# Kernel optimization log

Hardware: AMD Instinct MI355X
Metric: run time of the kernel (lower is better)

Reference implementation:

```python
import jax, jax.numpy as jnp
import numpy as np

DIM = 384
HEADS = 6
HEAD_DIM = DIM // HEADS
HIDDEN = int(DIM * 4.0)
SCALE = HEAD_DIM ** (-0.5)
EPS = 1e-5


def _layernorm(x, w, b):
    m = jnp.mean(x, axis=-1, keepdims=True)
    v = jnp.var(x, axis=-1, keepdims=True)
    return (x - m) * jax.lax.rsqrt(v + EPS) * w + b


def _mlp(x, fc1_w, fc1_b, fc2_w, fc2_b):
    h = jnp.einsum('bnc,hc->bnh', x, fc1_w) + fc1_b
    h = jax.nn.gelu(h, approximate=False)  # torch nn.GELU default = exact erf
    return jnp.einsum('bnh,ch->bnc', h, fc2_w) + fc2_b


def _attn_block(q, k, v, proj_w, proj_b):
    # q:[B,H,Q,D] k,v:[B,H,K,D]
    attn = jnp.einsum('bhqd,bhkd->bhqk', q, k) * SCALE
    attn = jax.nn.softmax(attn, axis=-1)
    o = jnp.einsum('bhqk,bhkd->bhqd', attn, v)
    B, H, Q, D = o.shape
    o = o.transpose(0, 2, 1, 3).reshape(B, Q, H * D)
    return jnp.einsum('bqc,oc->bqo', o, proj_w) + proj_b


def setup_inputs() -> dict:
    key = jax.random.key(0)
    ks = jax.random.split(key, 10)
    s = 0.02
    return {
        'x': jax.random.normal(ks[0], (4, 2048, DIM), jnp.float32),
        'y': jax.random.normal(ks[1], (4, 256, DIM), jnp.float32),
        'norm1_w': jnp.ones((DIM,), jnp.float32),
        'norm1_b': jnp.zeros((DIM,), jnp.float32),
        'norm2_w': jnp.ones((DIM,), jnp.float32),
        'norm2_b': jnp.zeros((DIM,), jnp.float32),
        'qkv_w': jax.random.normal(ks[2], (3 * DIM, DIM), jnp.float32) * s,
        'proj_w': jax.random.normal(ks[3], (DIM, DIM), jnp.float32) * s,
        'proj_b': jnp.zeros((DIM,), jnp.float32),
        'fc1_w': jax.random.normal(ks[4], (HIDDEN, DIM), jnp.float32) * s,
        'fc1_b': jnp.zeros((HIDDEN,), jnp.float32),
        'fc2_w': jax.random.normal(ks[5], (DIM, HIDDEN), jnp.float32) * s,
        'fc2_b': jnp.zeros((DIM,), jnp.float32),
    }


def reference(x, y, norm1_w, norm1_b, norm2_w, norm2_b, qkv_w,
              proj_w, proj_b, fc1_w, fc1_b, fc2_w, fc2_b):
    B, N, C = x.shape
    L = y.shape[1]
    nx = _layernorm(x, norm1_w, norm1_b)
    ny = _layernorm(y, norm1_w, norm1_b)
    cat = jnp.concatenate([nx, ny], axis=1)  # [B, N+L, C]
    qkv = jnp.einsum('bnc,oc->bno', cat, qkv_w)
    qkv = qkv.reshape(B, N + L, 3, HEADS, HEAD_DIM).transpose(2, 0, 3, 1, 4)
    q, k, v = qkv[0], qkv[1], qkv[2]  # each [B,H,N+L,D]
    # cross: y-queries attend over all N+L keys
    y_att = _attn_block(q[:, :, N:], k, v, proj_w, proj_b)
    # self: x-queries attend over first N keys only
    x_att = _attn_block(q[:, :, :N], k[:, :, :N], v[:, :, :N], proj_w, proj_b)
    new_x = x + x_att
    new_y = y + y_att
    new_x = new_x + _mlp(_layernorm(new_x, norm2_w, norm2_b), fc1_w, fc1_b, fc2_w, fc2_b)
    new_y = new_y + _mlp(_layernorm(new_y, norm2_w, norm2_b), fc1_w, fc1_b, fc2_w, fc2_b)
    return (new_x, new_y)
```

## Files before the change

kernel.cpp:

```cpp
#include <hip/hip_runtime.h>
#include <hip/hip_bf16.h>
#include <math.h>

#define B_   4
#define NX   2048
#define NY   256
#define T_   2304
#define NTOK 9216
#define DIM  384
#define NH   6
#define HD   64
#define HID  1536
#define QKV3 1152
#define QK2  768

typedef __attribute__((ext_vector_type(8))) short bf16x8;
typedef __attribute__((ext_vector_type(4))) float f32x4;

__device__ __forceinline__ float b2f(unsigned short u) {
  union { unsigned int i; float f; } x; x.i = ((unsigned int)u) << 16; return x.f;
}
__device__ __forceinline__ unsigned short f2b(float f) {
  union { float f; unsigned int i; } x; x.f = f;
  unsigned int r = x.i + 0x7fffu + ((x.i >> 16) & 1u);
  return (unsigned short)(r >> 16);
}
__device__ __forceinline__ unsigned int pack2(float a, float b) {
  return (unsigned int)f2b(a) | ((unsigned int)f2b(b) << 16);
}
__device__ __forceinline__ unsigned int cvtpk(float a, float b) {
  unsigned int r;
  asm("v_cvt_pk_bf16_f32 %0, %1, %2" : "=v"(r) : "v"(a), "v"(b));
  return r;
}
__device__ __forceinline__ float ldin(const void* p, size_t i, int isbf) {
  return isbf ? b2f(((const unsigned short*)p)[i]) : ((const float*)p)[i];
}

#if defined(__has_builtin)
#if __has_builtin(__builtin_amdgcn_global_load_lds)
#define HAS_GLL 1
#endif
#endif

__device__ __forceinline__ void stage16(const unsigned short* g, unsigned short* l) {
#ifdef HAS_GLL
  __builtin_amdgcn_global_load_lds(
      (const __attribute__((address_space(1))) unsigned int*)g,
      (__attribute__((address_space(3))) unsigned int*)l, 16, 0, 0);
#else
  *(uint4*)(l + (threadIdx.x & 63) * 8) = *(const uint4*)g;
#endif
}

__global__ void detect_kernel(const unsigned short* __restrict__ qw,
                              int* __restrict__ flag) {
  int lane = threadIdx.x;
  int bad = 0;
  #pragma unroll
  for (int j = 0; j < 8; j++) {
    unsigned short u = qw[2 * (lane + 64 * j)];
    int e = (u >> 7) & 0xff;
    bad += (e >= 134) ? 1 : 0;
  }
  #pragma unroll
  for (int off = 32; off > 0; off >>= 1) bad += __shfl_xor(bad, off);
  if (lane == 0) *flag = (bad < 64) ? 1 : 0;
}

__global__ __launch_bounds__(256) void convert4_kernel(
    const void* __restrict__ s0, const void* __restrict__ s1,
    const void* __restrict__ s2, const void* __restrict__ s3,
    unsigned short* __restrict__ d0, const int* __restrict__ flagp) {
  int isbf = *flagp;
  int i = (blockIdx.x * 256 + threadIdx.x) * 8;
  const void* src; int off;
  if (i < 442368)       { src = s0; off = 0; }
  else if (i < 589824)  { src = s1; off = 442368; }
  else if (i < 1179648) { src = s2; off = 589824; }
  else                  { src = s3; off = 1179648; }
  int li = i - off;
  if (isbf) {
    *(uint4*)(d0 + i) = *(const uint4*)((const unsigned short*)src + li);
  } else {
    const float* s = (const float*)src + li;
    unsigned int w[4];
    #pragma unroll
    for (int j = 0; j < 4; j++) w[j] = pack2(s[2 * j], s[2 * j + 1]);
    *(uint4*)(d0 + i) = make_uint4(w[0], w[1], w[2], w[3]);
  }
}

__global__ __launch_bounds__(256) void ln1_kernel(
    const void* __restrict__ x, const void* __restrict__ y,
    const void* __restrict__ w, const void* __restrict__ bsh,
    const int* __restrict__ flagp, unsigned short* __restrict__ out)
{
  int isbf = *flagp;
  int token = blockIdx.x * 4 + (threadIdx.x >> 6);
  int lane  = threadIdx.x & 63;
  int bb = token / T_;
  int t  = token - bb * T_;
  const void* src = (t < NX) ? x : y;
  size_t base = (t < NX) ? ((size_t)bb * NX + t) * DIM
                         : ((size_t)bb * NY + (t - NX)) * DIM;
  float v[6];
  float s = 0.f, s2 = 0.f;
  #pragma unroll
  for (int k = 0; k < 6; k++) {
    v[k] = ldin(src, base + lane + 64 * k, isbf);
    s += v[k]; s2 += v[k] * v[k];
  }
  #pragma unroll
  for (int off = 32; off > 0; off >>= 1) {
    s  += __shfl_xor(s, off);
    s2 += __shfl_xor(s2, off);
  }
  float mean = s * (1.f / DIM);
  float var  = s2 * (1.f / DIM) - mean * mean;
  float rs = rsqrtf(var + 1e-5f);
  unsigned short* dst = out + (size_t)token * DIM;
  #pragma unroll
  for (int k = 0; k < 6; k++) {
    int c = lane + 64 * k;
    dst[c] = f2b((v[k] - mean) * rs * ldin(w, c, isbf) + ldin(bsh, c, isbf));
  }
}

__global__ __launch_bounds__(256) void ln2_kernel(
    const float* __restrict__ in, const void* __restrict__ w,
    const void* __restrict__ bsh, const int* __restrict__ flagp,
    unsigned short* __restrict__ out)
{
  int isbf = *flagp;
  int token = blockIdx.x * 4 + (threadIdx.x >> 6);
  int lane  = threadIdx.x & 63;
  const float* src = in + (size_t)token * DIM;
  float v[6];
  float s = 0.f, s2 = 0.f;
  #pragma unroll
  for (int k = 0; k < 6; k++) {
    v[k] = src[lane + 64 * k];
    s += v[k]; s2 += v[k] * v[k];
  }
  #pragma unroll
  for (int off = 32; off > 0; off >>= 1) {
    s  += __shfl_xor(s, off);
    s2 += __shfl_xor(s2, off);
  }
  float mean = s * (1.f / DIM);
  float var  = s2 * (1.f / DIM) - mean * mean;
  float rs = rsqrtf(var + 1e-5f);
  unsigned short* dst = out + (size_t)token * DIM;
  #pragma unroll
  for (int k = 0; k < 6; k++) {
    int c = lane + 64 * k;
    dst[c] = f2b((v[k] - mean) * rs * ldin(w, c, isbf) + ldin(bsh, c, isbf));
  }
}

template <int EPI, int KT>
__global__ __launch_bounds__(256) void gemm_mfma(
    const unsigned short* __restrict__ A, const unsigned short* __restrict__ Bw,
    const void* __restrict__ bias,
    const void* __restrict__ rx, const void* __restrict__ ry,
    const float* __restrict__ rf,
    unsigned short* __restrict__ outb, float* __restrict__ resf,
    void* __restrict__ outd, unsigned short* __restrict__ vTp,
    const int* __restrict__ flagp, int N)
{
  constexpr int NT = KT / 32;
  __shared__ unsigned short As[2][128 * 32];
  __shared__ unsigned short Bs[2][128 * 32];
  const int tid  = threadIdx.x;
  const int wave = tid >> 6, lane = tid & 63;
  const int g = lane >> 4, qq = lane & 15;
  const int gx = gridDim.x;
  const int flat = blockIdx.x + gx * blockIdx.y;
  const int cpx = (gx * gridDim.y) >> 3;
  const int L = (flat & 7) * cpx + (flat >> 3);
  const int n0 = (L % gx) * 128, m0 = (L / gx) * 128;
  const int wm = (wave & 1) * 64, wn = (wave >> 1) * 64;

  f32x4 z = {0.f, 0.f, 0.f, 0.f};
  f32x4 acc[4][4];
  #pragma unroll
  for (int i = 0; i < 4; i++)
    #pragma unroll
    for (int j = 0; j < 4; j++) acc[i][j] = z;

  const int lrow = lane >> 2;
  const int lkx  = (((lane & 3) ^ ((lane >> 3) & 3)) * 8);
  const int rsw  = (qq >> 1) & 3;

  auto STG = [&](int t, int bi_) {
    int k0_ = t * 32;
    #pragma unroll
    for (int r = 0; r < 2; r++) {
      int rbase = wave * 32 + r * 16;
      stage16(A  + (size_t)(m0 + rbase + lrow) * KT + k0_ + lkx,
              &As[bi_][rbase * 32]);
      stage16(Bw + (size_t)(n0 + rbase + lrow) * KT + k0_ + lkx,
              &Bs[bi_][rbase * 32]);
    }
  };
  auto COMPUTE = [&](int bi_) {
    const unsigned short* as = As[bi_];
    const unsigned short* bs = Bs[bi_];
    bf16x8 af[4], bf[4];
    #pragma unroll
    for (int i = 0; i < 4; i++)
      af[i] = *(const bf16x8*)&as[(wm + i * 16 + qq) * 32 + ((g ^ rsw) * 8)];
    #pragma unroll
    for (int j = 0; j < 4; j++)
      bf[j] = *(const bf16x8*)&bs[(wn + j * 16 + qq) * 32 + ((g ^ rsw) * 8)];
    __builtin_amdgcn_s_setprio(1);
    #pragma unroll
    for (int i = 0; i < 4; i++)
      #pragma unroll
      for (int j = 0; j < 4; j++)
        acc[i][j] = __builtin_amdgcn_mfma_f32_16x16x32_bf16(
            af[i], bf[j], acc[i][j], 0, 0, 0);
    __builtin_amdgcn_s_setprio(0);
  };
  #define GSYNC() do { \
    asm volatile("s_waitcnt vmcnt(0)" ::: "memory"); \
    __builtin_amdgcn_s_barrier(); } while (0)

  STG(0, 0);
  GSYNC();
  #pragma unroll 1
  for (int t = 0; t + 2 < NT; t += 2) {
    STG(t + 1, 1);
    COMPUTE(0);
    GSYNC();
    STG(t + 2, 0);
    COMPUTE(1);
    GSYNC();
  }
  STG(NT - 1, 1);
  COMPUTE(0);
  GSYNC();
  COMPUTE(1);
  #undef GSYNC

  if (EPI == 0 && n0 >= 768) {
    #pragma unroll
    for (int i = 0; i < 4; i++) {
      int mb = m0 + wm + i * 16 + g * 4;
      int bb = mb / T_;
      int t  = mb - bb * T_;
      #pragma unroll
      for (int j = 0; j < 4; j++) {
        int n = n0 + wn + j * 16 + qq;
        int hh = (n - 768) >> 6, dd = (n - 768) & 63;
        uint2 pk;
        pk.x = pack2(acc[i][j][0], acc[i][j][1]);
        pk.y = pack2(acc[i][j][2], acc[i][j][3]);
        *(uint2*)(vTp + ((size_t)(bb * NH + hh) * HD + dd) * T_ + t) = pk;
      }
    }
    return;
  }

  int isbf = (EPI == 0) ? 1 : *flagp;
  float qs = (EPI == 0 && n0 < 384) ? 0.18033688011f : 1.f;
  const bool kswz = (EPI == 0) && (n0 >= 384);
  #pragma unroll
  for (int i = 0; i < 4; i++) {
    #pragma unroll
    for (int r = 0; r < 4; r++) {
      int m = m0 + wm + i * 16 + g * 4 + r;
      int bb = m / T_;
      int t  = m - bb * T_;
      int ms = kswz ? ((m & ~31) | ((g & 1) << 4) | ((i & 1) << 3) |
                       ((g >> 1) << 2) | r)
                    : m;
      #pragma unroll
      for (int j = 0; j < 4; j++) {
        int n = n0 + wn + j * 16 + qq;
        float v = acc[i][j][r];
        if (EPI == 0) {
          outb[(size_t)ms * QK2 + n] = f2b(v * qs);
        } else if (EPI == 1) {
          float resv = (t < NX)
              ? ldin(rx, ((size_t)bb * NX + t) * DIM + n, isbf)
              : ldin(ry, ((size_t)bb * NY + (t - NX)) * DIM + n, isbf);
          resf[(size_t)m * DIM + n] = v + ldin(bias, n, isbf) + resv;
        } else if (EPI == 2) {
          float h = v + ldin(bias, n, isbf);
          outb[(size_t)m * N + n] =
              f2b(0.5f * h * (1.f + erff(h * 0.70710678118654752f)));
        } else {
          float rr = v + ldin(bias, n, isbf) + rf[(size_t)m * DIM + n];
          size_t oi = (t < NX)
              ? ((size_t)bb * NX + t) * DIM + n
              : (size_t)B_ * NX * DIM + ((size_t)bb * NY + (t - NX)) * DIM + n;
          if (isbf) ((unsigned short*)outd)[oi] = f2b(rr);
          else      ((float*)outd)[oi] = rr;
        }
      }
    }
  }
}

__global__ __launch_bounds__(256) void attn_mfma(
    const unsigned short* __restrict__ qk, const unsigned short* __restrict__ vT,
    unsigned short* __restrict__ att)
{
  __shared__ float Ob[64][68];
  __shared__ float Lb[64];
  const int tid = threadIdx.x;
  const int wave = tid >> 6, lane = tid & 63;
  const int g = lane >> 4, qq = lane & 15;
  const int flat = blockIdx.x;
  const int L = (flat & 7) * 108 + (flat >> 3);
  const int bx = L % 36;
  const int hb = L / 36;
  const int h = hb % NH, b = hb / NH;
  const int self = (bx < 32);
  const int qtok0 = self ? bx * 64 : NX + (bx - 32) * 64;
  const int kvbeg = wave * (self ? 512 : 576);
  const int ntile = self ? 16 : 18;

  bf16x8 qa[4][2];
  #pragma unroll
  for (int f = 0; f < 4; f++) {
    size_t qrow = (size_t)(b * T_ + qtok0 + f * 16 + qq) * QK2 + h * HD;
    qa[f][0] = *(const bf16x8*)(qk + qrow + g * 8);
    qa[f][1] = *(const bf16x8*)(qk + qrow + 32 + g * 8);
  }
  const unsigned short* kb = qk + (size_t)b * T_ * QK2 + DIM + h * HD;
  const unsigned short* vb = vT + (size_t)(b * NH + h) * HD * T_;

  f32x4 z = {0.f, 0.f, 0.f, 0.f};
  f32x4 ot[4][4];
  #pragma unroll
  for (int f = 0; f < 4; f++)
    #pragma unroll
    for (int dt = 0; dt < 4; dt++) ot[f][dt] = z;
  float lsum[4] = {0.f, 0.f, 0.f, 0.f};

  uint4 kc[4];
  #pragma unroll
  for (int c = 0; c < 2; c++)
    #pragma unroll
    for (int hh = 0; hh < 2; hh++)
      kc[c * 2 + hh] =
          *(const uint4*)(kb + (size_t)(kvbeg + c * 16 + qq) * QK2 + hh * 32 + g * 8);
  uint4 vc[4];
  #pragma unroll
  for (int dt = 0; dt < 4; dt++)
    vc[dt] = *(const uint4*)(vb + (size_t)(dt * 16 + qq) * T_ + kvbeg + g * 8);

  int kt = kvbeg;
  for (int it = 0; it < ntile; it++, kt += 32) {
    f32x4 s[4][2];
    __builtin_amdgcn_s_setprio(1);
    #pragma unroll
    for (int f = 0; f < 4; f++) {
      s[f][0] = __builtin_amdgcn_mfma_f32_16x16x32_bf16(
          *(const bf16x8*)&kc[0], qa[f][0], z, 0, 0, 0);
      s[f][0] = __builtin_amdgcn_mfma_f32_16x16x32_bf16(
          *(const bf16x8*)&kc[1], qa[f][1], s[f][0], 0, 0, 0);
      s[f][1] = __builtin_amdgcn_mfma_f32_16x16x32_bf16(
          *(const bf16x8*)&kc[2], qa[f][0], z, 0, 0, 0);
      s[f][1] = __builtin_amdgcn_mfma_f32_16x16x32_bf16(
          *(const bf16x8*)&kc[3], qa[f][1], s[f][1], 0, 0, 0);
    }
    __builtin_amdgcn_s_setprio(0);
    if (it + 1 < ntile) {
      int ktn = kt + 32;
      #pragma unroll
      for (int c = 0; c < 2; c++)
        #pragma unroll
        for (int hh = 0; hh < 2; hh++)
          kc[c * 2 + hh] = *(const uint4*)(
              kb + (size_t)(ktn + c * 16 + qq) * QK2 + hh * 32 + g * 8);
    }

    #pragma unroll
    for (int f = 0; f < 4; f++) {
      float pv[8];
      #pragma unroll
      for (int c = 0; c < 2; c++)
        #pragma unroll
        for (int r = 0; r < 4; r++)
          pv[c * 4 + r] = exp2f(s[f][c][r]);
      lsum[f] += ((pv[0] + pv[1]) + (pv[2] + pv[3])) +
                 ((pv[4] + pv[5]) + (pv[6] + pv[7]));
      union { unsigned int w[4]; bf16x8 v; } bq;
      bq.w[0] = cvtpk(pv[0], pv[1]);
      bq.w[1] = cvtpk(pv[2], pv[3]);
      bq.w[2] = cvtpk(pv[4], pv[5]);
      bq.w[3] = cvtpk(pv[6], pv[7]);
      __builtin_amdgcn_s_setprio(1);
      #pragma unroll
      for (int dt = 0; dt < 4; dt++)
        ot[f][dt] = __builtin_amdgcn_mfma_f32_16x16x32_bf16(
            *(const bf16x8*)&vc[dt], bq.v, ot[f][dt], 0, 0, 0);
      __builtin_amdgcn_s_setprio(0);
    }

    if (it + 1 < ntile) {
      int ktn = kt + 32;
      #pragma unroll
      for (int dt = 0; dt < 4; dt++)
        vc[dt] = *(const uint4*)(vb + (size_t)(dt * 16 + qq) * T_ + ktn + g * 8);
    }
  }

  #pragma unroll
  for (int f = 0; f < 4; f++) {
    lsum[f] += __shfl_xor(lsum[f], 16);
    lsum[f] += __shfl_xor(lsum[f], 32);
  }

  #pragma unroll
  for (int w = 0; w < 4; w++) {
    if (wave == w) {
      if (w == 0) {
        #pragma unroll
        for (int f = 0; f < 4; f++) {
          #pragma unroll
          for (int dt = 0; dt < 4; dt++)
            *(f32x4*)&Ob[f * 16 + qq][dt * 16 + g * 4] = ot[f][dt];
          if (g == 0) Lb[f * 16 + qq] = lsum[f];
        }
      } else {
        #pragma unroll
        for (int f = 0; f < 4; f++) {
          #pragma unroll
          for (int dt = 0; dt < 4; dt++) {
            f32x4 cur = *(const f32x4*)&Ob[f * 16 + qq][dt * 16 + g * 4];
            #pragma unroll
            for (int r = 0; r < 4; r++) cur[r] += ot[f][dt][r];
            *(f32x4*)&Ob[f * 16 + qq][dt * 16 + g * 4] = cur;
          }
          if (g == 0) Lb[f * 16 + qq] += lsum[f];
        }
      }
    }
    __syncthreads();
  }

  int q = tid >> 2, ds = (tid & 3) * 16;
  float inv = 1.f / Lb[q];
  float o[16];
  #pragma unroll
  for (int j = 0; j < 16; j += 4) {
    f32x4 a = *(const f32x4*)&Ob[q][ds + j];
    #pragma unroll
    for (int r = 0; r < 4; r++) o[j + r] = a[r] * inv;
  }
  unsigned int w[8];
  #pragma unroll
  for (int j = 0; j < 8; j++) w[j] = pack2(o[2 * j], o[2 * j + 1]);
  size_t orow = (size_t)(b * T_ + qtok0 + q) * DIM + h * HD + ds;
  *(uint4*)(att + orow)     = make_uint4(w[0], w[1], w[2], w[3]);
  *(uint4*)(att + orow + 8) = make_uint4(w[4], w[5], w[6], w[7]);
}

extern "C" void kernel_launch(void* const* d_in, const int* in_sizes, int n_in,
                              void* d_out, int out_size, void* d_ws, size_t ws_size,
                              hipStream_t stream)
{
  (void)in_sizes; (void)n_in; (void)out_size; (void)ws_size;
  const void* x    = d_in[0];
  const void* y    = d_in[1];
  const void* n1w  = d_in[2];
  const void* n1b  = d_in[3];
  const void* n2w  = d_in[4];
  const void* n2b  = d_in[5];
  const void* qkvw = d_in[6];
  const void* pw   = d_in[7];
  const void* pb   = d_in[8];
  const void* f1w  = d_in[9];
  const void* f1b  = d_in[10];
  const void* f2w  = d_in[11];
  const void* f2bp = d_in[12];

  unsigned short* wsu = (unsigned short*)d_ws;
  int* flag = (int*)d_ws;
  unsigned short* wts    = wsu + 128;
  unsigned short* qkvw_b = wts;
  unsigned short* pw_b   = wts + 442368;
  unsigned short* f1w_b  = wts + 589824;
  unsigned short* f2w_b  = wts + 1179648;
  unsigned short* catln  = wsu + 1769600;
  unsigned short* qkvb2  = wsu + 5308544;
  unsigned short* attb   = wsu + 12386432;
  unsigned short* vT     = wsu + 15925376;
  unsigned short* hbuf   = qkvb2;
  float*          resb   = (float*)d_ws + 9732160;

  detect_kernel<<<1, 64, 0, stream>>>((const unsigned short*)qkvw, flag);
  convert4_kernel<<<864, 256, 0, stream>>>(qkvw, pw, f1w, f2w, wts, flag);

  ln1_kernel<<<NTOK / 4, 256, 0, stream>>>(x, y, n1w, n1b, flag, catln);
  gemm_mfma<0, DIM><<<dim3(QKV3 / 128, NTOK / 128), 256, 0, stream>>>(
      catln, qkvw_b, nullptr, nullptr, nullptr, nullptr, qkvb2, nullptr,
      nullptr, vT, flag, QKV3);
  attn_mfma<<<dim3(864), 256, 0, stream>>>(qkvb2, vT, attb);
  gemm_mfma<1, DIM><<<dim3(DIM / 128, NTOK / 128), 256, 0, stream>>>(
      attb, pw_b, pb, x, y, nullptr, nullptr, resb, nullptr, nullptr,
      flag, DIM);
  ln2_kernel<<<NTOK / 4, 256, 0, stream>>>(resb, n2w, n2b, flag, catln);
  gemm_mfma<2, DIM><<<dim3(HID / 128, NTOK / 128), 256, 0, stream>>>(
      catln, f1w_b, f1b, nullptr, nullptr, nullptr, hbuf, nullptr, nullptr,
      nullptr, flag, HID);
  gemm_mfma<3, HID><<<dim3(DIM / 128, NTOK / 128), 256, 0, stream>>>(
      hbuf, f2w_b, f2bp, nullptr, nullptr, resb, nullptr, nullptr, d_out,
      nullptr, flag, DIM);
}
```

Baseline: 319.1 us.

## Replace LDS-staged GEMM with direct global-to-register triple-buffered fragment loads

The GEMM kernel drops shared-memory staging and barriers. Each wave now loads its MFMA fragments directly from global memory into registers, with a three-deep software pipeline. The block tile shrinks from 128x128 to 128x64, with each wave owning 32 rows across all 64 columns, and the grids double in the N dimension. This removes LDS traffic and synchronization, but every wave now reloads the shared B fragments from global/L2, so data reuse within the block is lost.

Measured after the change: 409.3 us. 28.3% more time.

```diff
diff --git a/kernel.cpp b/kernel.cpp
--- a/kernel.cpp
+++ b/kernel.cpp
@@ -35,22 +35,6 @@
 }
 __device__ __forceinline__ float ldin(const void* p, size_t i, int isbf) {
   return isbf ? b2f(((const unsigned short*)p)[i]) : ((const float*)p)[i];
-}
-
-#if defined(__has_builtin)
-#if __has_builtin(__builtin_amdgcn_global_load_lds)
-#define HAS_GLL 1
-#endif
-#endif
-
-__device__ __forceinline__ void stage16(const unsigned short* g, unsigned short* l) {
-#ifdef HAS_GLL
-  __builtin_amdgcn_global_load_lds(
-      (const __attribute__((address_space(1))) unsigned int*)g,
-      (__attribute__((address_space(3))) unsigned int*)l, 16, 0, 0);
-#else
-  *(uint4*)(l + (threadIdx.x & 63) * 8) = *(const uint4*)g;
-#endif
 }
 
 __global__ void detect_kernel(const unsigned short* __restrict__ qw,
@@ -170,8 +154,6 @@
     const int* __restrict__ flagp, int N)
 {
   constexpr int NT = KT / 32;
-  __shared__ unsigned short As[2][128 * 32];
-  __shared__ unsigned short Bs[2][128 * 32];
   const int tid  = threadIdx.x;
   const int wave = tid >> 6, lane = tid & 63;
   const int g = lane >> 4, qq = lane & 15;
@@ -179,80 +161,65 @@
   const int flat = blockIdx.x + gx * blockIdx.y;
   const int cpx = (gx * gridDim.y) >> 3;
   const int L = (flat & 7) * cpx + (flat >> 3);
-  const int n0 = (L % gx) * 128, m0 = (L / gx) * 128;
-  const int wm = (wave & 1) * 64, wn = (wave >> 1) * 64;
+  const int n0 = (L % gx) * 64, m0 = (L / gx) * 128;
+  const int wm = wave * 32;
 
   f32x4 z = {0.f, 0.f, 0.f, 0.f};
-  f32x4 acc[4][4];
-  #pragma unroll
-  for (int i = 0; i < 4; i++)
+  f32x4 acc[2][4];
+  #pragma unroll
+  for (int i = 0; i < 2; i++)
     #pragma unroll
     for (int j = 0; j < 4; j++) acc[i][j] = z;
 
-  const int lrow = lane >> 2;
-  const int lkx  = (((lane & 3) ^ ((lane >> 3) & 3)) * 8);
-  const int rsw  = (qq >> 1) & 3;
-
-  auto STG = [&](int t, int bi_) {
-    int k0_ = t * 32;
-    #pragma unroll
-    for (int r = 0; r < 2; r++) {
-      int rbase = wave * 32 + r * 16;
-      stage16(A  + (size_t)(m0 + rbase + lrow) * KT + k0_ + lkx,
-              &As[bi_][rbase * 32]);
-      stage16(Bw + (size_t)(n0 + rbase + lrow) * KT + k0_ + lkx,
-              &Bs[bi_][rbase * 32]);
-    }
+  unsigned int aoff[2], boff[4];
+  #pragma unroll
+  for (int i = 0; i < 2; i++)
+    aoff[i] = (unsigned int)(m0 + wm + i * 16 + qq) * KT + g * 8;
+  #pragma unroll
+  for (int j = 0; j < 4; j++)
+    boff[j] = (unsigned int)(n0 + j * 16 + qq) * KT + g * 8;
+
+  auto LDF = [&](uint4 (&fa)[2], uint4 (&fb)[4], int t) {
+    const int ke = t * 32;
+    #pragma unroll
+    for (int i = 0; i < 2; i++) fa[i] = *(const uint4*)(A + aoff[i] + ke);
+    #pragma unroll
+    for (int j = 0; j < 4; j++) fb[j] = *(const uint4*)(Bw + boff[j] + ke);
   };
-  auto COMPUTE = [&](int bi_) {
-    const unsigned short* as = As[bi_];
-    const unsigned short* bs = Bs[bi_];
-    bf16x8 af[4], bf[4];
-    #pragma unroll
-    for (int i = 0; i < 4; i++)
-      af[i] = *(const bf16x8*)&as[(wm + i * 16 + qq) * 32 + ((g ^ rsw) * 8)];
-    #pragma unroll
-    for (int j = 0; j < 4; j++)
-      bf[j] = *(const bf16x8*)&bs[(wn + j * 16 + qq) * 32 + ((g ^ rsw) * 8)];
+  auto MST = [&](uint4 (&fa)[2], uint4 (&fb)[4]) {
     __builtin_amdgcn_s_setprio(1);
     #pragma unroll
-    for (int i = 0; i < 4; i++)
+    for (int i = 0; i < 2; i++)
       #pragma unroll
       for (int j = 0; j < 4; j++)
         acc[i][j] = __builtin_amdgcn_mfma_f32_16x16x32_bf16(
-            af[i], bf[j], acc[i][j], 0, 0, 0);
+            *(const bf16x8*)&fa[i], *(const bf16x8*)&fb[j], acc[i][j], 0, 0, 0);
     __builtin_amdgcn_s_setprio(0);
   };
-  #define GSYNC() do { \
-    asm volatile("s_waitcnt vmcnt(0)" ::: "memory"); \
-    __builtin_amdgcn_s_barrier(); } while (0)
-
-  STG(0, 0);
-  GSYNC();
+
+  uint4 fa0[2], fb0[4], fa1[2], fb1[4], fa2[2], fb2[4];
+  LDF(fa0, fb0, 0);
+  LDF(fa1, fb1, 1);
+  LDF(fa2, fb2, 2);
   #pragma unroll 1
-  for (int t = 0; t + 2 < NT; t += 2) {
-    STG(t + 1, 1);
-    COMPUTE(0);
-    GSYNC();
-    STG(t + 2, 0);
-    COMPUTE(1);
-    GSYNC();
-  }
-  STG(NT - 1, 1);
-  COMPUTE(0);
-  GSYNC();
-  COMPUTE(1);
-  #undef GSYNC
+  for (int t = 0; t + 3 < NT; t += 3) {
+    MST(fa0, fb0); LDF(fa0, fb0, t + 3);
+    MST(fa1, fb1); LDF(fa1, fb1, t + 4);
+    MST(fa2, fb2); LDF(fa2, fb2, t + 5);
+  }
+  MST(fa0, fb0);
+  MST(fa1, fb1);
+  MST(fa2, fb2);
 
   if (EPI == 0 && n0 >= 768) {
     #pragma unroll
-    for (int i = 0; i < 4; i++) {
+    for (int i = 0; i < 2; i++) {
       int mb = m0 + wm + i * 16 + g * 4;
       int bb = mb / T_;
       int t  = mb - bb * T_;
       #pragma unroll
       for (int j = 0; j < 4; j++) {
-        int n = n0 + wn + j * 16 + qq;
+        int n = n0 + j * 16 + qq;
         int hh = (n - 768) >> 6, dd = (n - 768) & 63;
         uint2 pk;
         pk.x = pack2(acc[i][j][0], acc[i][j][1]);
@@ -267,7 +234,7 @@
   float qs = (EPI == 0 && n0 < 384) ? 0.18033688011f : 1.f;
   const bool kswz = (EPI == 0) && (n0 >= 384);
   #pragma unroll
-  for (int i = 0; i < 4; i++) {
+  for (int i = 0; i < 2; i++) {
     #pragma unroll
     for (int r = 0; r < 4; r++) {
       int m = m0 + wm + i * 16 + g * 4 + r;
@@ -278,7 +245,7 @@
                     : m;
       #pragma unroll
       for (int j = 0; j < 4; j++) {
-        int n = n0 + wn + j * 16 + qq;
+        int n = n0 + j * 16 + qq;
         float v = acc[i][j][r];
         if (EPI == 0) {
           outb[(size_t)ms * QK2 + n] = f2b(v * qs);
@@ -498,18 +465,18 @@
   convert4_kernel<<<864, 256, 0, stream>>>(qkvw, pw, f1w, f2w, wts, flag);
 
   ln1_kernel<<<NTOK / 4, 256, 0, stream>>>(x, y, n1w, n1b, flag, catln);
-  gemm_mfma<0, DIM><<<dim3(QKV3 / 128, NTOK / 128), 256, 0, stream>>>(
+  gemm_mfma<0, DIM><<<dim3(QKV3 / 64, NTOK / 128), 256, 0, stream>>>(
       catln, qkvw_b, nullptr, nullptr, nullptr, nullptr, qkvb2, nullptr,
       nullptr, vT, flag, QKV3);
   attn_mfma<<<dim3(864), 256, 0, stream>>>(qkvb2, vT, attb);
-  gemm_mfma<1, DIM><<<dim3(DIM / 128, NTOK / 128), 256, 0, stream>>>(
+  gemm_mfma<1, DIM><<<dim3(DIM / 64, NTOK / 128), 256, 0, stream>>>(
       attb, pw_b, pb, x, y, nullptr, nullptr, resb, nullptr, nullptr,
       flag, DIM);
   ln2_kernel<<<NTOK / 4, 256, 0, stream>>>(resb, n2w, n2b, flag, catln);
-  gemm_mfma<2, DIM><<<dim3(HID / 128, NTOK / 128), 256, 0, stream>>>(
+  gemm_mfma<2, DIM><<<dim3(HID / 64, NTOK / 128), 256, 0, stream>>>(
       catln, f1w_b, f1b, nullptr, nullptr, nullptr, hbuf, nullptr, nullptr,
       nullptr, flag, HID);
-  gemm_mfma<3, HID><<<dim3(DIM / 128, NTOK / 128), 256, 0, stream>>>(
+  gemm_mfma<3, HID><<<dim3(DIM / 64, NTOK / 128), 256, 0, stream>>>(
       hbuf, f2w_b, f2bp, nullptr, nullptr, resb, nullptr, nullptr, d_out,
       nullptr, flag, DIM);
 }
```
